# Kernel optimization log

Hardware: AMD Instinct MI355X
Metric: run time of the kernel (lower is better)

The kernel has to match this reference:

```python
import jax, jax.numpy as jnp
import numpy as np

D_MODEL = 1024
NUM_HEADS = 16
HEAD_DIM = D_MODEL // NUM_HEADS
BATCH = 2
SEQ = 2048


def setup_inputs() -> dict:
    key = jax.random.key(0)
    ks = jax.random.split(key, 9)
    s = 1.0 / np.sqrt(D_MODEL)
    X = jax.random.normal(ks[0], (BATCH, SEQ, D_MODEL), dtype=jnp.float32)
    # causal mask, broadcastable over batch and heads; masked_fill where mask == 0
    mask = jnp.tril(jnp.ones((SEQ, SEQ), dtype=jnp.int32))[None, None, :, :]
    Wq = jax.random.uniform(ks[1], (D_MODEL, D_MODEL), jnp.float32, -s, s)
    bq = jax.random.uniform(ks[2], (D_MODEL,), jnp.float32, -s, s)
    Wk = jax.random.uniform(ks[3], (D_MODEL, D_MODEL), jnp.float32, -s, s)
    bk = jax.random.uniform(ks[4], (D_MODEL,), jnp.float32, -s, s)
    Wv = jax.random.uniform(ks[5], (D_MODEL, D_MODEL), jnp.float32, -s, s)
    bv = jax.random.uniform(ks[6], (D_MODEL,), jnp.float32, -s, s)
    Wo = jax.random.uniform(ks[7], (D_MODEL, D_MODEL), jnp.float32, -s, s)
    bo = jax.random.uniform(ks[8], (D_MODEL,), jnp.float32, -s, s)
    return {"X": X, "mask": mask, "Wq": Wq, "bq": bq, "Wk": Wk, "bk": bk,
            "Wv": Wv, "bv": bv, "Wo": Wo, "bo": bo}


def reference(X, mask, Wq, bq, Wk, bk, Wv, bv, Wo, bo):
    B, S, _ = X.shape
    scale = 1.0 / np.sqrt(HEAD_DIM).astype(np.float32)

    def split_heads(t):  # [B,S,D] -> [B,H,S,Dh]
        return t.reshape(B, S, NUM_HEADS, HEAD_DIM).transpose(0, 2, 1, 3)

    q = split_heads(X @ Wq.T + bq)
    k = split_heads(X @ Wk.T + bk)
    v = split_heads(X @ Wv.T + bv)
    # [B,H,S,S] attention logits (explicitly materialized, as in the source)
    logits = jnp.einsum("bhqd,bhkd->bhqk", q, k) * scale
    logits = jnp.where(mask == 0, -jnp.inf, logits)
    attn = jax.nn.softmax(logits, axis=-1)  # dropout in eval mode: identity
    ctx = jnp.einsum("bhqk,bhkd->bhqd", attn, v)
    ctx = ctx.transpose(0, 2, 1, 3).reshape(B, S, D_MODEL)
    return ctx @ Wo.T + bo
```

## Files before the change

kernel.cpp:

```cpp
#include <hip/hip_runtime.h>


#define B_   2
#define S_   2048
#define H_   16
#define DH_  64
#define D_   1024
#define M_   (B_ * S_)

typedef __attribute__((ext_vector_type(8))) short short8;
typedef __attribute__((ext_vector_type(4))) short short4_t;
typedef float v4f __attribute__((ext_vector_type(4)));

__device__ __forceinline__ short f2bf(float f) {
    union { float f; unsigned u; } v; v.f = f;
    unsigned r = v.u + 0x7fffu + ((v.u >> 16) & 1u);
    return (short)(r >> 16);
}

#if __has_builtin(__builtin_amdgcn_exp2f)
#define EXP2(x) __builtin_amdgcn_exp2f(x)
#else
#define EXP2(x) exp2f(x)
#endif

__device__ __forceinline__ unsigned pack2(float a, float b) {
    return (__float_as_uint(a) >> 16) | (__float_as_uint(b) & 0xFFFF0000u);
}

__device__ __forceinline__ void gl2lds16(const short* g, short* l) {
    __builtin_amdgcn_global_load_lds(
        (const __attribute__((address_space(1))) unsigned int*)g,
        (__attribute__((address_space(3))) unsigned int*)l,
        16, 0, 0);
}

__global__ __launch_bounds__(256) void cast_kernel(
    const float* __restrict__ X,
    const float* __restrict__ Wq, const float* __restrict__ Wk,
    const float* __restrict__ Wv, const float* __restrict__ Wo,
    short* __restrict__ Xb, short* __restrict__ Wb)
{
    const int NX8 = (M_ * D_) / 8;
    const int NW8 = (D_ * D_) / 8;
    int idx = blockIdx.x * 256 + threadIdx.x;

    const float* src; short* dst; int off;
    if (idx < NX8) { src = X; dst = Xb; off = idx; }
    else {
        int r = idx - NX8;
        int sel = r >> 17;
        int o = r & (NW8 - 1);
        src = (sel == 0) ? Wq : (sel == 1) ? Wk : (sel == 2) ? Wv : Wo;
        dst = Wb + sel * (D_ * D_);
        off = o;
    }
    float4 f0 = ((const float4*)src)[off * 2];
    float4 f1 = ((const float4*)src)[off * 2 + 1];
    short8 s;
    s[0] = f2bf(f0.x); s[1] = f2bf(f0.y); s[2] = f2bf(f0.z); s[3] = f2bf(f0.w);
    s[4] = f2bf(f1.x); s[5] = f2bf(f1.y); s[6] = f2bf(f1.z); s[7] = f2bf(f1.w);
    *(short8*)(dst + (size_t)off * 8) = s;
}

template<int BN, int MODE>
__global__ __launch_bounds__(256) void gemm_kernel(
    const short* __restrict__ A, const short* __restrict__ W,
    const float* __restrict__ bq, const float* __restrict__ bk,
    const float* __restrict__ bv, void* __restrict__ out,
    int M, int N, int K)
{
    constexpr int SM = (MODE == 0) ? 18432 : (8192 + BN * 64);
    __shared__ __align__(16) short smem[SM];
    short* As = smem;
    short* Bs = smem + 8192;

    const int t    = threadIdx.x;
    const int lane = t & 63;
    const int wave = t >> 6;

    const int bid = blockIdx.x;
    const int by  = ((bid & 7) << 2) + ((bid >> 3) & 3);
    const int bx  = bid >> 5;
    const int m0 = by * 128;
    const int n0 = bx * BN;

    const int wm = (wave >> 1) * 64;
    const int wn = (wave & 1) * (BN / 2);
    constexpr int NJ  = BN / 32;
    constexpr int BIT = BN / 32;

    v4f acc[4][NJ] = {};

    const int rsub = lane >> 3;
    const int csw  = ((lane & 7) ^ rsub) * 8;
    const short* Ag = A + (size_t)(m0 + wave * 32 + rsub) * K + csw;
    const short* Wg = W + (size_t)(n0 + wave * (BN / 4) + rsub) * K + csw;
    short* Asw = As + (wave * 32) * 64;
    short* Bsw = Bs + (wave * (BN / 4)) * 64;

    const int lm = lane & 15;
    const int lg = lane >> 4;
    const int lm7 = lm & 7;

    for (int k0 = 0; k0 < K; k0 += 64) {
        #pragma unroll
        for (int i2 = 0; i2 < 4; ++i2)
            gl2lds16(Ag + (size_t)(i2 * 8) * K + k0, Asw + i2 * 512);
        #pragma unroll
        for (int i2 = 0; i2 < BIT; ++i2)
            gl2lds16(Wg + (size_t)(i2 * 8) * K + k0, Bsw + i2 * 512);
        __syncthreads();

        #pragma unroll
        for (int kk = 0; kk < 2; ++kk) {
            const int ch = (kk * 4 + lg) ^ lm7;
            short8 af[4], bf[NJ];
            #pragma unroll
            for (int i = 0; i < 4; ++i)
                af[i] = *(const short8*)((const char*)As + (wm + i * 16 + lm) * 128 + ch * 16);
            #pragma unroll
            for (int j = 0; j < NJ; ++j)
                bf[j] = *(const short8*)((const char*)Bs + (wn + j * 16 + lm) * 128 + ch * 16);
            #pragma unroll
            for (int i = 0; i < 4; ++i)
                #pragma unroll
                for (int j = 0; j < NJ; ++j)
                    acc[i][j] = __builtin_amdgcn_mfma_f32_16x16x32_bf16(af[i], bf[j], acc[i][j], 0, 0, 0);
        }
        __syncthreads();
    }

    const int sel = n0 >> 10;
    const float* bias = (MODE == 2) ? bq : (sel == 0) ? bq : (sel == 1) ? bk : bv;

    if constexpr (MODE == 2) {
        const int colb = n0 + wn + lm;
        const int rowb = m0 + wm + lg * 4;
        #pragma unroll
        for (int j = 0; j < NJ; ++j) {
            int col = colb + j * 16;
            float bv_ = bias[col];
            #pragma unroll
            for (int i = 0; i < 4; ++i)
                #pragma unroll
                for (int r = 0; r < 4; ++r)
                    ((float*)out)[(size_t)(rowb + i * 16 + r) * 1024 + col] = acc[i][j][r] + bv_;
        }
    } else {
        short* Es = smem + wave * (64 * 72);
        const int cb = (n0 + wn) & 1023;
        #pragma unroll
        for (int j = 0; j < 4; ++j) {
            float bv_ = bias[cb + j * 16 + lm];
            #pragma unroll
            for (int i = 0; i < 4; ++i)
                #pragma unroll
                for (int r = 0; r < 4; ++r) {
                    float vv = acc[i][j][r] + bv_;
                    if (sel == 0) vv *= 0.1803368867f;
                    if (sel < 2)
                        Es[(i * 16 + lg * 4 + r) * 72 + j * 16 + lm] = f2bf(vv);
                    else
                        Es[(j * 16 + lm) * 72 + i * 16 + lg * 4 + r] = f2bf(vv);
                }
        }
        __asm__ __volatile__("s_waitcnt lgkmcnt(0)" ::: "memory");
        short* outQKV = (short*)out;
        const int rl = lane >> 3;
        const int c8 = (lane & 7) * 8;
        const int h  = cb >> 6;
        const int b  = (m0 + wm) >> 11;
        const int bh = (b << 4) + h;
        if (sel < 2) {
            #pragma unroll
            for (int it = 0; it < 8; ++it) {
                int row_l = it * 8 + rl;
                short8 vrow = *(const short8*)&Es[row_l * 72 + c8];
                int s = (m0 + wm + row_l) & 2047;
                *(short8*)(outQKV + (size_t)sel * 4194304 +
                           ((size_t)bh * S_ + s) * DH_ + c8) = vrow;
            }
        } else {
            const int s0 = (m0 + wm) & 2047;
            #pragma unroll
            for (int it = 0; it < 8; ++it) {
                int d_l = it * 8 + rl;
                short8 vrow = *(const short8*)&Es[d_l * 72 + c8];
                *(short8*)(outQKV + (size_t)2 * 4194304 +
                           ((size_t)bh << 17) + ((size_t)d_l << 11) + s0 + c8) = vrow;
            }
        }
    }
}

__global__ __launch_bounds__(256, 2) void attn_kernel(
    const short* __restrict__ Q, const short* __restrict__ Kh,
    const short* __restrict__ Vt, short* __restrict__ ctx)
{
    __shared__ __align__(16) short sm[16384];
    short* Kt = sm;
    short* Vp = sm + 8192;

    const int t    = threadIdx.x;
    const int lane = t & 63;
    const int w    = t >> 6;
    const int bid  = blockIdx.x;

    const int lo  = bid & 255;
    const int xcd = lo & 7;
    const int idx = lo >> 3;
    const int bh  = (xcd << 2) + (idx & 3);
    const int jb  = idx >> 2;
    const int j   = (bid < 256) ? jb : (15 - jb);
    const int q0  = j * 128;
    const int npairs = j + 1;
    const int qr0 = q0 + w * 32;

    const int lm = lane & 15;
    const int lg = lane >> 4;

    const short* Qb = Q  + (size_t)bh * S_ * DH_;
    const short* Kb = Kh + (size_t)bh * S_ * DH_;
    const short* Vb = Vt + ((size_t)bh << 17);

    short8 qf[2][2];
    #pragma unroll
    for (int t2 = 0; t2 < 2; ++t2)
        #pragma unroll
        for (int kk = 0; kk < 2; ++kk)
            qf[t2][kk] = *(const short8*)(Qb + (size_t)(qr0 + t2 * 16 + lm) * DH_ + kk * 32 + lg * 8);

    float m_i[2] = {-1e30f, -1e30f}, l_i[2] = {0.f, 0.f};
    v4f o[2][4] = {};

    for (int it = 0; it < npairs; ++it) {
        const int kv0 = it * 128;
        const bool dpair = (it == npairs - 1);

        {
            const int rsub = lane >> 3;
            const int csw  = ((lane & 7) ^ rsub) * 8;
            #pragma unroll
            for (int i2 = 0; i2 < 4; ++i2) {
                const int rb = w * 32 + i2 * 8;
                gl2lds16(Kb + (size_t)(kv0 + rb + rsub) * 64 + csw, Kt + rb * 64);
            }
        }
        {
            const int d  = w * 16 + (lane >> 2);
            const int s3 = d & 7;
            short8 vld[4];
            #pragma unroll
            for (int m = 0; m < 4; ++m) {
                const int cm = (lane & 3) + 4 * m;
                vld[m] = *(const short8*)(Vb + (size_t)d * 2048 + kv0 + cm * 8);
            }
            char* vrow = (char*)Vp + d * 256;
            #pragma unroll
            for (int m = 0; m < 4; ++m) {
                const int cm = (lane & 3) + 4 * m;
                const int u  = cm >> 3, kk = (cm >> 2) & 1;
                const int q0off = ((cm & 1) << 4) + ((cm >> 1) & 1) * 4;
                const int bA = (u * 64 + kk * 32 + q0off) * 2;
                const int pA = ((((bA >> 4) ^ s3) << 4) | (bA & 15));
                const int bB = bA + 16;
                const int pB = ((((bB >> 4) ^ s3) << 4) | (bB & 15));
                *(short4_t*)(vrow + pA) = __builtin_shufflevector(vld[m], vld[m], 0, 1, 2, 3);
                *(short4_t*)(vrow + pB) = __builtin_shufflevector(vld[m], vld[m], 4, 5, 6, 7);
            }
        }
        __syncthreads();

        short8 vf[2][2][4];
        #pragma unroll
        for (int u = 0; u < 2; ++u)
            #pragma unroll
            for (int kk = 0; kk < 2; ++kk)
                #pragma unroll
                for (int i = 0; i < 4; ++i) {
                    const int d = i * 16 + lm;
                    const int ch = (u * 8 + kk * 4 + lg) ^ (lm & 7);
                    vf[u][kk][i] = *(const short8*)((const char*)Vp + d * 256 + ch * 16);
                }

        v4f sc[2][2][4] = {};
        #pragma unroll
        for (int u = 0; u < 2; ++u) {
            short8 kf[2][4];
            #pragma unroll
            for (int kk = 0; kk < 2; ++kk)
                #pragma unroll
                for (int jj = 0; jj < 4; ++jj) {
                    const int row = u * 64 + jj * 16 + lm;
                    const int ch  = (kk * 4 + lg) ^ (lm & 7);
                    kf[kk][jj] = *(const short8*)((const char*)Kt + row * 128 + ch * 16);
                }
            #pragma unroll
            for (int kk = 0; kk < 2; ++kk)
                #pragma unroll
                for (int t2 = 0; t2 < 2; ++t2)
                    #pragma unroll
                    for (int jj = 0; jj < 4; ++jj)
                        sc[t2][u][jj] = __builtin_amdgcn_mfma_f32_16x16x32_bf16(kf[kk][jj], qf[t2][kk], sc[t2][u][jj], 0, 0, 0);
        }

        float alpha[2];
        short8 pf[2][2][2];
        #pragma unroll
        for (int t2 = 0; t2 < 2; ++t2) {
            float x[2][4][4];
            const int q = qr0 + t2 * 16 + lm;
            #pragma unroll
            for (int u = 0; u < 2; ++u)
                #pragma unroll
                for (int jj = 0; jj < 4; ++jj)
                    #pragma unroll
                    for (int r = 0; r < 4; ++r) {
                        float v = sc[t2][u][jj][r];
                        if (dpair && (kv0 + u * 64 + jj * 16 + lg * 4 + r > q)) v = -1e30f;
                        x[u][jj][r] = v;
                    }
            float m8[8];
            #pragma unroll
            for (int z = 0; z < 8; ++z) {
                const float* xz = x[z >> 2][z & 3];
                m8[z] = fmaxf(fmaxf(xz[0], xz[1]), fmaxf(xz[2], xz[3]));
            }
            float rm = fmaxf(fmaxf(fmaxf(m8[0], m8[1]), fmaxf(m8[2], m8[3])),
                             fmaxf(fmaxf(m8[4], m8[5]), fmaxf(m8[6], m8[7])));
            rm = fmaxf(rm, __shfl_xor(rm, 16, 64));
            rm = fmaxf(rm, __shfl_xor(rm, 32, 64));

            const float mn = fmaxf(m_i[t2], rm);
            alpha[t2] = EXP2(m_i[t2] - mn);
            m_i[t2] = mn;

            float s8[8];
            #pragma unroll
            for (int z = 0; z < 8; ++z) {
                float* xz = x[z >> 2][z & 3];
                xz[0] = EXP2(xz[0] - mn); xz[1] = EXP2(xz[1] - mn);
                xz[2] = EXP2(xz[2] - mn); xz[3] = EXP2(xz[3] - mn);
                s8[z] = (xz[0] + xz[1]) + (xz[2] + xz[3]);
            }
            float rs = ((s8[0] + s8[1]) + (s8[2] + s8[3])) + ((s8[4] + s8[5]) + (s8[6] + s8[7]));
            rs += __shfl_xor(rs, 16, 64);
            rs += __shfl_xor(rs, 32, 64);
            l_i[t2] = l_i[t2] * alpha[t2] + rs;

            #pragma unroll
            for (int u = 0; u < 2; ++u)
                #pragma unroll
                for (int kk = 0; kk < 2; ++kk) {
                    union { short8 s; uint4 d; } pk;
                    pk.d.x = pack2(x[u][2 * kk][0],     x[u][2 * kk][1]);
                    pk.d.y = pack2(x[u][2 * kk][2],     x[u][2 * kk][3]);
                    pk.d.z = pack2(x[u][2 * kk + 1][0], x[u][2 * kk + 1][1]);
                    pk.d.w = pack2(x[u][2 * kk + 1][2], x[u][2 * kk + 1][3]);
                    pf[t2][u][kk] = pk.s;
                }
        }

        #pragma unroll
        for (int t2 = 0; t2 < 2; ++t2)
            #pragma unroll
            for (int i = 0; i < 4; ++i)
                o[t2][i] *= alpha[t2];

        #pragma unroll
        for (int u = 0; u < 2; ++u)
            #pragma unroll
            for (int kk = 0; kk < 2; ++kk)
                #pragma unroll
                for (int t2 = 0; t2 < 2; ++t2)
                    #pragma unroll
                    for (int i = 0; i < 4; ++i)
                        o[t2][i] = __builtin_amdgcn_mfma_f32_16x16x32_bf16(vf[u][kk][i], pf[t2][u][kk], o[t2][i], 0, 0, 0);

        __syncthreads();
    }

    const int b = bh >> 4, hd = bh & 15;
    #pragma unroll
    for (int t2 = 0; t2 < 2; ++t2) {
        const float inv = 1.f / l_i[t2];
        const size_t base = ((size_t)(b * S_ + qr0 + t2 * 16 + lm) << 10) + (hd << 6) + lg * 4;
        #pragma unroll
        for (int i = 0; i < 4; ++i) {
            short4_t s4;
            #pragma unroll
            for (int r = 0; r < 4; ++r) s4[r] = f2bf(o[t2][i][r] * inv);
            *(short4_t*)(ctx + base + i * 16) = s4;
        }
    }
}

extern "C" void kernel_launch(void* const* d_in, const int* in_sizes, int n_in,
                              void* d_out, int out_size, void* d_ws, size_t ws_size,
                              hipStream_t stream) {
    const float* X  = (const float*)d_in[0];
    const float* Wq = (const float*)d_in[2];
    const float* bq = (const float*)d_in[3];
    const float* Wk = (const float*)d_in[4];
    const float* bk = (const float*)d_in[5];
    const float* Wv = (const float*)d_in[6];
    const float* bv = (const float*)d_in[7];
    const float* Wo = (const float*)d_in[8];
    const float* bo = (const float*)d_in[9];
    float* out = (float*)d_out;

    short* ws  = (short*)d_ws;
    short* Xb  = ws;
    short* Wb  = Xb + 4194304;
    short* Qh  = Wb + 4194304;
    short* Kb  = Qh + 4194304;
    short* Vt  = Kb + 4194304;
    short* Ctx = Vt + 4194304;

    cast_kernel<<<4096, 256, 0, stream>>>(X, Wq, Wk, Wv, Wo, Xb, Wb);

    gemm_kernel<128, 0><<<768, 256, 0, stream>>>(
        Xb, Wb, bq, bk, bv, Qh, M_, 3 * D_, D_);

    attn_kernel<<<512, 256, 0, stream>>>(Qh, Kb, Vt, Ctx);

    gemm_kernel<64, 2><<<512, 256, 0, stream>>>(
        Ctx, Wb + 3145728, bo, bo, bo, out, M_, D_, D_);
}
```

Baseline: 195.8 us.

## Double-buffer K/V tiles in LDS to prefetch next block during compute

Doubles the attention kernel's shared memory to two K/V buffers and issues the next block's K async copy and V global loads before computing the current block. V is written into the alternate buffer after the MFMA work, so each iteration needs one barrier instead of two and load latency can overlap compute. The cost is 64KB of LDS per block, which may limit occupancy at 2 blocks per CU, plus extra registers held for the prefetched V.

```diff
diff --git a/kernel.cpp b/kernel.cpp
--- a/kernel.cpp
+++ b/kernel.cpp
@@ -198,9 +198,7 @@
     const short* __restrict__ Q, const short* __restrict__ Kh,
     const short* __restrict__ Vt, short* __restrict__ ctx)
 {
-    __shared__ __align__(16) short sm[16384];
-    short* Kt = sm;
-    short* Vp = sm + 8192;
+    __shared__ __align__(16) short sm[32768];
 
     const int t    = threadIdx.x;
     const int lane = t & 63;
@@ -224,6 +222,41 @@
     const short* Kb = Kh + (size_t)bh * S_ * DH_;
     const short* Vb = Vt + ((size_t)bh << 17);
 
+    const int rsubK = lane >> 3;
+    const int cswK  = ((lane & 7) ^ rsubK) * 8;
+    const int dV    = w * 16 + (lane >> 2);
+    const int s3V   = dV & 7;
+
+    auto stageK = [&](int kv0, short* Kt) {
+        #pragma unroll
+        for (int i2 = 0; i2 < 4; ++i2) {
+            const int rb = w * 32 + i2 * 8;
+            gl2lds16(Kb + (size_t)(kv0 + rb + rsubK) * 64 + cswK, Kt + rb * 64);
+        }
+    };
+    auto loadV = [&](int kv0, short8* vld) {
+        #pragma unroll
+        for (int m = 0; m < 4; ++m) {
+            const int cm = (lane & 3) + 4 * m;
+            vld[m] = *(const short8*)(Vb + (size_t)dV * 2048 + kv0 + cm * 8);
+        }
+    };
+    auto writeV = [&](const short8* vld, short* Vp) {
+        char* vrow = (char*)Vp + dV * 256;
+        #pragma unroll
+        for (int m = 0; m < 4; ++m) {
+            const int cm = (lane & 3) + 4 * m;
+            const int u  = cm >> 3, kk = (cm >> 2) & 1;
+            const int q0off = ((cm & 1) << 4) + ((cm >> 1) & 1) * 4;
+            const int bA = (u * 64 + kk * 32 + q0off) * 2;
+            const int pA = ((((bA >> 4) ^ s3V) << 4) | (bA & 15));
+            const int bB = bA + 16;
+            const int pB = ((((bB >> 4) ^ s3V) << 4) | (bB & 15));
+            *(short4_t*)(vrow + pA) = __builtin_shufflevector(vld[m], vld[m], 0, 1, 2, 3);
+            *(short4_t*)(vrow + pB) = __builtin_shufflevector(vld[m], vld[m], 4, 5, 6, 7);
+        }
+    };
+
     short8 qf[2][2];
     #pragma unroll
     for (int t2 = 0; t2 < 2; ++t2)
@@ -234,43 +267,26 @@
     float m_i[2] = {-1e30f, -1e30f}, l_i[2] = {0.f, 0.f};
     v4f o[2][4] = {};
 
+    short8 vpre[4];
+    stageK(0, sm);
+    loadV(0, vpre);
+    writeV(vpre, sm + 8192);
+    __syncthreads();
+
+    int cur = 0;
     for (int it = 0; it < npairs; ++it) {
         const int kv0 = it * 128;
         const bool dpair = (it == npairs - 1);
-
-        {
-            const int rsub = lane >> 3;
-            const int csw  = ((lane & 7) ^ rsub) * 8;
-            #pragma unroll
-            for (int i2 = 0; i2 < 4; ++i2) {
-                const int rb = w * 32 + i2 * 8;
-                gl2lds16(Kb + (size_t)(kv0 + rb + rsub) * 64 + csw, Kt + rb * 64);
-            }
-        }
-        {
-            const int d  = w * 16 + (lane >> 2);
-            const int s3 = d & 7;
-            short8 vld[4];
-            #pragma unroll
-            for (int m = 0; m < 4; ++m) {
-                const int cm = (lane & 3) + 4 * m;
-                vld[m] = *(const short8*)(Vb + (size_t)d * 2048 + kv0 + cm * 8);
-            }
-            char* vrow = (char*)Vp + d * 256;
-            #pragma unroll
-            for (int m = 0; m < 4; ++m) {
-                const int cm = (lane & 3) + 4 * m;
-                const int u  = cm >> 3, kk = (cm >> 2) & 1;
-                const int q0off = ((cm & 1) << 4) + ((cm >> 1) & 1) * 4;
-                const int bA = (u * 64 + kk * 32 + q0off) * 2;
-                const int pA = ((((bA >> 4) ^ s3) << 4) | (bA & 15));
-                const int bB = bA + 16;
-                const int pB = ((((bB >> 4) ^ s3) << 4) | (bB & 15));
-                *(short4_t*)(vrow + pA) = __builtin_shufflevector(vld[m], vld[m], 0, 1, 2, 3);
-                *(short4_t*)(vrow + pB) = __builtin_shufflevector(vld[m], vld[m], 4, 5, 6, 7);
-            }
-        }
-        __syncthreads();
+        const bool pre   = (it + 1 < npairs);
+        short* Kt  = sm + cur * 16384;
+        short* Vp  = Kt + 8192;
+        short* Ktn = sm + (cur ^ 1) * 16384;
+        short* Vpn = Ktn + 8192;
+
+        if (pre) {
+            stageK(kv0 + 128, Ktn);
+            loadV(kv0 + 128, vpre);
+        }
 
         short8 vf[2][2][4];
         #pragma unroll
@@ -378,7 +394,9 @@
                     for (int i = 0; i < 4; ++i)
                         o[t2][i] = __builtin_amdgcn_mfma_f32_16x16x32_bf16(vf[u][kk][i], pf[t2][u][kk], o[t2][i], 0, 0, 0);
 
+        if (pre) writeV(vpre, Vpn);
         __syncthreads();
+        cur ^= 1;
     }
 
     const int b = bh >> 4, hd = bh & 15;
```

Result: slower. 237.6 us (+21.4%).

## Split attention block across 8 waves with 16 query rows each

Applied to the files above, without the earlier changes.

The attention kernel now launches 512 threads (8 waves) per block instead of 256, and each wave handles 16 query rows instead of 32. The K and V tile loads into shared memory are redistributed across the 8 waves. This cuts per-thread registers and adds waves per CU to hide latency. In exchange, each wave re-reads the full K and V fragments from LDS for half as many queries, which doubles LDS read traffic per unit of work.

```diff
diff --git a/kernel.cpp b/kernel.cpp
--- a/kernel.cpp
+++ b/kernel.cpp
@@ -194,7 +194,7 @@
     }
 }
 
-__global__ __launch_bounds__(256, 2) void attn_kernel(
+__global__ __launch_bounds__(512, 2) void attn_kernel(
     const short* __restrict__ Q, const short* __restrict__ Kh,
     const short* __restrict__ Vt, short* __restrict__ ctx)
 {
@@ -215,7 +215,7 @@
     const int j   = (bid < 256) ? jb : (15 - jb);
     const int q0  = j * 128;
     const int npairs = j + 1;
-    const int qr0 = q0 + w * 32;
+    const int qr0 = q0 + w * 16;
 
     const int lm = lane & 15;
     const int lg = lane >> 4;
@@ -224,15 +224,13 @@
     const short* Kb = Kh + (size_t)bh * S_ * DH_;
     const short* Vb = Vt + ((size_t)bh << 17);
 
-    short8 qf[2][2];
+    short8 qf[2];
     #pragma unroll
-    for (int t2 = 0; t2 < 2; ++t2)
-        #pragma unroll
-        for (int kk = 0; kk < 2; ++kk)
-            qf[t2][kk] = *(const short8*)(Qb + (size_t)(qr0 + t2 * 16 + lm) * DH_ + kk * 32 + lg * 8);
-
-    float m_i[2] = {-1e30f, -1e30f}, l_i[2] = {0.f, 0.f};
-    v4f o[2][4] = {};
+    for (int kk = 0; kk < 2; ++kk)
+        qf[kk] = *(const short8*)(Qb + (size_t)(qr0 + lm) * DH_ + kk * 32 + lg * 8);
+
+    float m_i = -1e30f, l_i = 0.f;
+    v4f o[4] = {};
 
     for (int it = 0; it < npairs; ++it) {
         const int kv0 = it * 128;
@@ -242,24 +240,24 @@
             const int rsub = lane >> 3;
             const int csw  = ((lane & 7) ^ rsub) * 8;
             #pragma unroll
-            for (int i2 = 0; i2 < 4; ++i2) {
-                const int rb = w * 32 + i2 * 8;
+            for (int i2 = 0; i2 < 2; ++i2) {
+                const int rb = w * 16 + i2 * 8;
                 gl2lds16(Kb + (size_t)(kv0 + rb + rsub) * 64 + csw, Kt + rb * 64);
             }
         }
         {
-            const int d  = w * 16 + (lane >> 2);
+            const int d  = w * 8 + (lane >> 3);
             const int s3 = d & 7;
-            short8 vld[4];
-            #pragma unroll
-            for (int m = 0; m < 4; ++m) {
-                const int cm = (lane & 3) + 4 * m;
+            short8 vld[2];
+            #pragma unroll
+            for (int m = 0; m < 2; ++m) {
+                const int cm = (lane & 7) + 8 * m;
                 vld[m] = *(const short8*)(Vb + (size_t)d * 2048 + kv0 + cm * 8);
             }
             char* vrow = (char*)Vp + d * 256;
             #pragma unroll
-            for (int m = 0; m < 4; ++m) {
-                const int cm = (lane & 3) + 4 * m;
+            for (int m = 0; m < 2; ++m) {
+                const int cm = (lane & 7) + 8 * m;
                 const int u  = cm >> 3, kk = (cm >> 2) & 1;
                 const int q0off = ((cm & 1) << 4) + ((cm >> 1) & 1) * 4;
                 const int bA = (u * 64 + kk * 32 + q0off) * 2;
@@ -284,7 +282,7 @@
                     vf[u][kk][i] = *(const short8*)((const char*)Vp + d * 256 + ch * 16);
                 }
 
-        v4f sc[2][2][4] = {};
+        v4f sc[2][4] = {};
         #pragma unroll
         for (int u = 0; u < 2; ++u) {
             short8 kf[2][4];
@@ -299,25 +297,22 @@
             #pragma unroll
             for (int kk = 0; kk < 2; ++kk)
                 #pragma unroll
-                for (int t2 = 0; t2 < 2; ++t2)
-                    #pragma unroll
-                    for (int jj = 0; jj < 4; ++jj)
-                        sc[t2][u][jj] = __builtin_amdgcn_mfma_f32_16x16x32_bf16(kf[kk][jj], qf[t2][kk], sc[t2][u][jj], 0, 0, 0);
-        }
-
-        float alpha[2];
-        short8 pf[2][2][2];
-        #pragma unroll
-        for (int t2 = 0; t2 < 2; ++t2) {
+                for (int jj = 0; jj < 4; ++jj)
+                    sc[u][jj] = __builtin_amdgcn_mfma_f32_16x16x32_bf16(kf[kk][jj], qf[kk], sc[u][jj], 0, 0, 0);
+        }
+
+        float alpha;
+        short8 pf[2][2];
+        {
             float x[2][4][4];
-            const int q = qr0 + t2 * 16 + lm;
+            const int q = qr0 + lm;
             #pragma unroll
             for (int u = 0; u < 2; ++u)
                 #pragma unroll
                 for (int jj = 0; jj < 4; ++jj)
                     #pragma unroll
                     for (int r = 0; r < 4; ++r) {
-                        float v = sc[t2][u][jj][r];
+                        float v = sc[u][jj][r];
                         if (dpair && (kv0 + u * 64 + jj * 16 + lg * 4 + r > q)) v = -1e30f;
                         x[u][jj][r] = v;
                     }
@@ -332,9 +327,9 @@
             rm = fmaxf(rm, __shfl_xor(rm, 16, 64));
             rm = fmaxf(rm, __shfl_xor(rm, 32, 64));
 
-            const float mn = fmaxf(m_i[t2], rm);
-            alpha[t2] = EXP2(m_i[t2] - mn);
-            m_i[t2] = mn;
+            const float mn = fmaxf(m_i, rm);
+            alpha = EXP2(m_i - mn);
+            m_i = mn;
 
             float s8[8];
             #pragma unroll
@@ -347,7 +342,7 @@
             float rs = ((s8[0] + s8[1]) + (s8[2] + s8[3])) + ((s8[4] + s8[5]) + (s8[6] + s8[7]));
             rs += __shfl_xor(rs, 16, 64);
             rs += __shfl_xor(rs, 32, 64);
-            l_i[t2] = l_i[t2] * alpha[t2] + rs;
+            l_i = l_i * alpha + rs;
 
             #pragma unroll
             for (int u = 0; u < 2; ++u)
@@ -358,39 +353,34 @@
                     pk.d.y = pack2(x[u][2 * kk][2],     x[u][2 * kk][3]);
                     pk.d.z = pack2(x[u][2 * kk + 1][0], x[u][2 * kk + 1][1]);
                     pk.d.w = pack2(x[u][2 * kk + 1][2], x[u][2 * kk + 1][3]);
-                    pf[t2][u][kk] = pk.s;
+                    pf[u][kk] = pk.s;
                 }
         }
 
         #pragma unroll
-        for (int t2 = 0; t2 < 2; ++t2)
-            #pragma unroll
-            for (int i = 0; i < 4; ++i)
-                o[t2][i] *= alpha[t2];
+        for (int i = 0; i < 4; ++i)
+            o[i] *= alpha;
 
         #pragma unroll
         for (int u = 0; u < 2; ++u)
             #pragma unroll
             for (int kk = 0; kk < 2; ++kk)
                 #pragma unroll
-                for (int t2 = 0; t2 < 2; ++t2)
-                    #pragma unroll
-                    for (int i = 0; i < 4; ++i)
-                        o[t2][i] = __builtin_amdgcn_mfma_f32_16x16x32_bf16(vf[u][kk][i], pf[t2][u][kk], o[t2][i], 0, 0, 0);
+                for (int i = 0; i < 4; ++i)
+                    o[i] = __builtin_amdgcn_mfma_f32_16x16x32_bf16(vf[u][kk][i], pf[u][kk], o[i], 0, 0, 0);
 
         __syncthreads();
     }
 
     const int b = bh >> 4, hd = bh & 15;
-    #pragma unroll
-    for (int t2 = 0; t2 < 2; ++t2) {
-        const float inv = 1.f / l_i[t2];
-        const size_t base = ((size_t)(b * S_ + qr0 + t2 * 16 + lm) << 10) + (hd << 6) + lg * 4;
+    {
+        const float inv = 1.f / l_i;
+        const size_t base = ((size_t)(b * S_ + qr0 + lm) << 10) + (hd << 6) + lg * 4;
         #pragma unroll
         for (int i = 0; i < 4; ++i) {
             short4_t s4;
             #pragma unroll
-            for (int r = 0; r < 4; ++r) s4[r] = f2bf(o[t2][i][r] * inv);
+            for (int r = 0; r < 4; ++r) s4[r] = f2bf(o[i][r] * inv);
             *(short4_t*)(ctx + base + i * 16) = s4;
         }
     }
@@ -423,7 +413,7 @@
     gemm_kernel<128, 0><<<768, 256, 0, stream>>>(
         Xb, Wb, bq, bk, bv, Qh, M_, 3 * D_, D_);
 
-    attn_kernel<<<512, 256, 0, stream>>>(Qh, Kb, Vt, Ctx);
+    attn_kernel<<<512, 512, 0, stream>>>(Qh, Kb, Vt, Ctx);
 
     gemm_kernel<64, 2><<<512, 256, 0, stream>>>(
         Ctx, Wb + 3145728, bo, bo, bo, out, M_, D_, D_);
```

After: 191.1 us. 2.4% less time.

## Split attention KV range across two wave groups with in-block softmax merge

Applied to the files above, without the earlier changes.

The attention block grows from 256 to 512 threads. Two groups of four waves each process half of the causal KV tiles for the same 128 query rows, using separate shared-memory K/V buffers. At the end, group 1 writes its partial max, sum and output to LDS, and group 0 merges them with a log-sum-exp rescale before writing ctx. This doubles the waves working on each query tile to increase parallelism and latency hiding. In exchange it doubles LDS per block, may lower blocks per CU, and makes the inactive group idle at barriers when the tile count is odd.

```diff
diff --git a/kernel.cpp b/kernel.cpp
--- a/kernel.cpp
+++ b/kernel.cpp
@@ -194,17 +194,17 @@
     }
 }
 
-__global__ __launch_bounds__(256, 2) void attn_kernel(
+__global__ __launch_bounds__(512, 2) void attn_kernel(
     const short* __restrict__ Q, const short* __restrict__ Kh,
     const short* __restrict__ Vt, short* __restrict__ ctx)
 {
-    __shared__ __align__(16) short sm[16384];
-    short* Kt = sm;
-    short* Vp = sm + 8192;
+    __shared__ __align__(16) short sm[32768];
 
     const int t    = threadIdx.x;
     const int lane = t & 63;
     const int w    = t >> 6;
+    const int wg   = w & 3;
+    const int g    = w >> 2;
     const int bid  = blockIdx.x;
 
     const int lo  = bid & 255;
@@ -214,16 +214,28 @@
     const int jb  = idx >> 2;
     const int j   = (bid < 256) ? jb : (15 - jb);
     const int q0  = j * 128;
-    const int npairs = j + 1;
-    const int qr0 = q0 + w * 32;
+    const int nt  = j + 1;
+    const int ha  = nt >> 1;
+    const int mx  = nt - ha;
+    const int pb  = g ? ha : 0;
+    const int np  = g ? (nt - ha) : ha;
+    const int qr0 = q0 + wg * 32;
 
     const int lm = lane & 15;
     const int lg = lane >> 4;
+
+    short* Kt = sm + g * 16384;
+    short* Vp = Kt + 8192;
 
     const short* Qb = Q  + (size_t)bh * S_ * DH_;
     const short* Kb = Kh + (size_t)bh * S_ * DH_;
     const short* Vb = Vt + ((size_t)bh << 17);
 
+    const int rsubK = lane >> 3;
+    const int cswK  = ((lane & 7) ^ rsubK) * 8;
+    const int dV    = wg * 16 + (lane >> 2);
+    const int s3V   = dV & 7;
+
     short8 qf[2][2];
     #pragma unroll
     for (int t2 = 0; t2 < 2; ++t2)
@@ -234,164 +246,191 @@
     float m_i[2] = {-1e30f, -1e30f}, l_i[2] = {0.f, 0.f};
     v4f o[2][4] = {};
 
-    for (int it = 0; it < npairs; ++it) {
-        const int kv0 = it * 128;
-        const bool dpair = (it == npairs - 1);
-
-        {
-            const int rsub = lane >> 3;
-            const int csw  = ((lane & 7) ^ rsub) * 8;
+    for (int tI = 0; tI < mx; ++tI) {
+        const bool act   = tI < np;
+        const int  kv0   = (pb + tI) * 128;
+        const bool dpair = (g == 1) && (tI == mx - 1);
+
+        if (act) {
             #pragma unroll
             for (int i2 = 0; i2 < 4; ++i2) {
-                const int rb = w * 32 + i2 * 8;
-                gl2lds16(Kb + (size_t)(kv0 + rb + rsub) * 64 + csw, Kt + rb * 64);
-            }
-        }
-        {
-            const int d  = w * 16 + (lane >> 2);
-            const int s3 = d & 7;
+                const int rb = wg * 32 + i2 * 8;
+                gl2lds16(Kb + (size_t)(kv0 + rb + rsubK) * 64 + cswK, Kt + rb * 64);
+            }
             short8 vld[4];
             #pragma unroll
             for (int m = 0; m < 4; ++m) {
                 const int cm = (lane & 3) + 4 * m;
-                vld[m] = *(const short8*)(Vb + (size_t)d * 2048 + kv0 + cm * 8);
-            }
-            char* vrow = (char*)Vp + d * 256;
+                vld[m] = *(const short8*)(Vb + (size_t)dV * 2048 + kv0 + cm * 8);
+            }
+            char* vrow = (char*)Vp + dV * 256;
             #pragma unroll
             for (int m = 0; m < 4; ++m) {
                 const int cm = (lane & 3) + 4 * m;
                 const int u  = cm >> 3, kk = (cm >> 2) & 1;
                 const int q0off = ((cm & 1) << 4) + ((cm >> 1) & 1) * 4;
                 const int bA = (u * 64 + kk * 32 + q0off) * 2;
-                const int pA = ((((bA >> 4) ^ s3) << 4) | (bA & 15));
+                const int pA = ((((bA >> 4) ^ s3V) << 4) | (bA & 15));
                 const int bB = bA + 16;
-                const int pB = ((((bB >> 4) ^ s3) << 4) | (bB & 15));
+                const int pB = ((((bB >> 4) ^ s3V) << 4) | (bB & 15));
                 *(short4_t*)(vrow + pA) = __builtin_shufflevector(vld[m], vld[m], 0, 1, 2, 3);
                 *(short4_t*)(vrow + pB) = __builtin_shufflevector(vld[m], vld[m], 4, 5, 6, 7);
             }
         }
         __syncthreads();
 
-        short8 vf[2][2][4];
-        #pragma unroll
-        for (int u = 0; u < 2; ++u)
-            #pragma unroll
-            for (int kk = 0; kk < 2; ++kk)
-                #pragma unroll
-                for (int i = 0; i < 4; ++i) {
-                    const int d = i * 16 + lm;
-                    const int ch = (u * 8 + kk * 4 + lg) ^ (lm & 7);
-                    vf[u][kk][i] = *(const short8*)((const char*)Vp + d * 256 + ch * 16);
+        if (act) {
+            short8 vf[2][2][4];
+            #pragma unroll
+            for (int u = 0; u < 2; ++u)
+                #pragma unroll
+                for (int kk = 0; kk < 2; ++kk)
+                    #pragma unroll
+                    for (int i = 0; i < 4; ++i) {
+                        const int d = i * 16 + lm;
+                        const int ch = (u * 8 + kk * 4 + lg) ^ (lm & 7);
+                        vf[u][kk][i] = *(const short8*)((const char*)Vp + d * 256 + ch * 16);
+                    }
+
+            v4f sc[2][2][4] = {};
+            #pragma unroll
+            for (int u = 0; u < 2; ++u) {
+                short8 kf[2][4];
+                #pragma unroll
+                for (int kk = 0; kk < 2; ++kk)
+                    #pragma unroll
+                    for (int jj = 0; jj < 4; ++jj) {
+                        const int row = u * 64 + jj * 16 + lm;
+                        const int ch  = (kk * 4 + lg) ^ (lm & 7);
+                        kf[kk][jj] = *(const short8*)((const char*)Kt + row * 128 + ch * 16);
+                    }
+                #pragma unroll
+                for (int kk = 0; kk < 2; ++kk)
+                    #pragma unroll
+                    for (int t2 = 0; t2 < 2; ++t2)
+                        #pragma unroll
+                        for (int jj = 0; jj < 4; ++jj)
+                            sc[t2][u][jj] = __builtin_amdgcn_mfma_f32_16x16x32_bf16(kf[kk][jj], qf[t2][kk], sc[t2][u][jj], 0, 0, 0);
+            }
+
+            float alpha[2];
+            short8 pf[2][2][2];
+            #pragma unroll
+            for (int t2 = 0; t2 < 2; ++t2) {
+                float x[2][4][4];
+                const int q = qr0 + t2 * 16 + lm;
+                #pragma unroll
+                for (int u = 0; u < 2; ++u)
+                    #pragma unroll
+                    for (int jj = 0; jj < 4; ++jj)
+                        #pragma unroll
+                        for (int r = 0; r < 4; ++r) {
+                            float v = sc[t2][u][jj][r];
+                            if (dpair && (kv0 + u * 64 + jj * 16 + lg * 4 + r > q)) v = -1e30f;
+                            x[u][jj][r] = v;
+                        }
+                float m8[8];
+                #pragma unroll
+                for (int z = 0; z < 8; ++z) {
+                    const float* xz = x[z >> 2][z & 3];
+                    m8[z] = fmaxf(fmaxf(xz[0], xz[1]), fmaxf(xz[2], xz[3]));
                 }
-
-        v4f sc[2][2][4] = {};
-        #pragma unroll
-        for (int u = 0; u < 2; ++u) {
-            short8 kf[2][4];
-            #pragma unroll
-            for (int kk = 0; kk < 2; ++kk)
-                #pragma unroll
-                for (int jj = 0; jj < 4; ++jj) {
-                    const int row = u * 64 + jj * 16 + lm;
-                    const int ch  = (kk * 4 + lg) ^ (lm & 7);
-                    kf[kk][jj] = *(const short8*)((const char*)Kt + row * 128 + ch * 16);
+                float rm = fmaxf(fmaxf(fmaxf(m8[0], m8[1]), fmaxf(m8[2], m8[3])),
+                                 fmaxf(fmaxf(m8[4], m8[5]), fmaxf(m8[6], m8[7])));
+                rm = fmaxf(rm, __shfl_xor(rm, 16, 64));
+                rm = fmaxf(rm, __shfl_xor(rm, 32, 64));
+
+                const float mn = fmaxf(m_i[t2], rm);
+                alpha[t2] = EXP2(m_i[t2] - mn);
+                m_i[t2] = mn;
+
+                float s8[8];
+                #pragma unroll
+                for (int z = 0; z < 8; ++z) {
+                    float* xz = x[z >> 2][z & 3];
+                    xz[0] = EXP2(xz[0] - mn); xz[1] = EXP2(xz[1] - mn);
+                    xz[2] = EXP2(xz[2] - mn); xz[3] = EXP2(xz[3] - mn);
+                    s8[z] = (xz[0] + xz[1]) + (xz[2] + xz[3]);
                 }
-            #pragma unroll
-            for (int kk = 0; kk < 2; ++kk)
-                #pragma unroll
-                for (int t2 = 0; t2 < 2; ++t2)
-                    #pragma unroll
-                    for (int jj = 0; jj < 4; ++jj)
-                        sc[t2][u][jj] = __builtin_amdgcn_mfma_f32_16x16x32_bf16(kf[kk][jj], qf[t2][kk], sc[t2][u][jj], 0, 0, 0);
-        }
-
-        float alpha[2];
-        short8 pf[2][2][2];
+                float rs = ((s8[0] + s8[1]) + (s8[2] + s8[3])) + ((s8[4] + s8[5]) + (s8[6] + s8[7]));
+                rs += __shfl_xor(rs, 16, 64);
+                rs += __shfl_xor(rs, 32, 64);
+                l_i[t2] = l_i[t2] * alpha[t2] + rs;
+
+                #pragma unroll
+                for (int u = 0; u < 2; ++u)
+                    #pragma unroll
+                    for (int kk = 0; kk < 2; ++kk) {
+                        union { short8 s; uint4 d; } pk;
+                        pk.d.x = pack2(x[u][2 * kk][0],     x[u][2 * kk][1]);
+                        pk.d.y = pack2(x[u][2 * kk][2],     x[u][2 * kk][3]);
+                        pk.d.z = pack2(x[u][2 * kk + 1][0], x[u][2 * kk + 1][1]);
+                        pk.d.w = pack2(x[u][2 * kk + 1][2], x[u][2 * kk + 1][3]);
+                        pf[t2][u][kk] = pk.s;
+                    }
+            }
+
+            #pragma unroll
+            for (int t2 = 0; t2 < 2; ++t2)
+                #pragma unroll
+                for (int i = 0; i < 4; ++i)
+                    o[t2][i] *= alpha[t2];
+
+            #pragma unroll
+            for (int u = 0; u < 2; ++u)
+                #pragma unroll
+                for (int kk = 0; kk < 2; ++kk)
+                    #pragma unroll
+                    for (int t2 = 0; t2 < 2; ++t2)
+                        #pragma unroll
+                        for (int i = 0; i < 4; ++i)
+                            o[t2][i] = __builtin_amdgcn_mfma_f32_16x16x32_bf16(vf[u][kk][i], pf[t2][u][kk], o[t2][i], 0, 0, 0);
+        }
+        __syncthreads();
+    }
+
+    float* fb = (float*)sm;
+    if (g == 1) {
+        float* mp = &fb[(wg * 64 + lane) * 36];
+        mp[0] = m_i[0]; mp[1] = l_i[0]; mp[2] = m_i[1]; mp[3] = l_i[1];
+        #pragma unroll
+        for (int t2 = 0; t2 < 2; ++t2)
+            #pragma unroll
+            for (int i = 0; i < 4; ++i)
+                #pragma unroll
+                for (int r = 0; r < 4; ++r)
+                    mp[4 + t2 * 16 + i * 4 + r] = o[t2][i][r];
+    }
+    __syncthreads();
+    if (g == 0) {
+        const float* mp = &fb[(wg * 64 + lane) * 36];
         #pragma unroll
         for (int t2 = 0; t2 < 2; ++t2) {
-            float x[2][4][4];
-            const int q = qr0 + t2 * 16 + lm;
-            #pragma unroll
-            for (int u = 0; u < 2; ++u)
-                #pragma unroll
-                for (int jj = 0; jj < 4; ++jj)
-                    #pragma unroll
-                    for (int r = 0; r < 4; ++r) {
-                        float v = sc[t2][u][jj][r];
-                        if (dpair && (kv0 + u * 64 + jj * 16 + lg * 4 + r > q)) v = -1e30f;
-                        x[u][jj][r] = v;
-                    }
-            float m8[8];
-            #pragma unroll
-            for (int z = 0; z < 8; ++z) {
-                const float* xz = x[z >> 2][z & 3];
-                m8[z] = fmaxf(fmaxf(xz[0], xz[1]), fmaxf(xz[2], xz[3]));
-            }
-            float rm = fmaxf(fmaxf(fmaxf(m8[0], m8[1]), fmaxf(m8[2], m8[3])),
-                             fmaxf(fmaxf(m8[4], m8[5]), fmaxf(m8[6], m8[7])));
-            rm = fmaxf(rm, __shfl_xor(rm, 16, 64));
-            rm = fmaxf(rm, __shfl_xor(rm, 32, 64));
-
-            const float mn = fmaxf(m_i[t2], rm);
-            alpha[t2] = EXP2(m_i[t2] - mn);
-            m_i[t2] = mn;
-
-            float s8[8];
-            #pragma unroll
-            for (int z = 0; z < 8; ++z) {
-                float* xz = x[z >> 2][z & 3];
-                xz[0] = EXP2(xz[0] - mn); xz[1] = EXP2(xz[1] - mn);
-                xz[2] = EXP2(xz[2] - mn); xz[3] = EXP2(xz[3] - mn);
-                s8[z] = (xz[0] + xz[1]) + (xz[2] + xz[3]);
-            }
-            float rs = ((s8[0] + s8[1]) + (s8[2] + s8[3])) + ((s8[4] + s8[5]) + (s8[6] + s8[7]));
-            rs += __shfl_xor(rs, 16, 64);
-            rs += __shfl_xor(rs, 32, 64);
-            l_i[t2] = l_i[t2] * alpha[t2] + rs;
-
-            #pragma unroll
-            for (int u = 0; u < 2; ++u)
-                #pragma unroll
-                for (int kk = 0; kk < 2; ++kk) {
-                    union { short8 s; uint4 d; } pk;
-                    pk.d.x = pack2(x[u][2 * kk][0],     x[u][2 * kk][1]);
-                    pk.d.y = pack2(x[u][2 * kk][2],     x[u][2 * kk][3]);
-                    pk.d.z = pack2(x[u][2 * kk + 1][0], x[u][2 * kk + 1][1]);
-                    pk.d.w = pack2(x[u][2 * kk + 1][2], x[u][2 * kk + 1][3]);
-                    pf[t2][u][kk] = pk.s;
-                }
-        }
-
-        #pragma unroll
-        for (int t2 = 0; t2 < 2; ++t2)
-            #pragma unroll
-            for (int i = 0; i < 4; ++i)
-                o[t2][i] *= alpha[t2];
-
-        #pragma unroll
-        for (int u = 0; u < 2; ++u)
-            #pragma unroll
-            for (int kk = 0; kk < 2; ++kk)
-                #pragma unroll
-                for (int t2 = 0; t2 < 2; ++t2)
-                    #pragma unroll
-                    for (int i = 0; i < 4; ++i)
-                        o[t2][i] = __builtin_amdgcn_mfma_f32_16x16x32_bf16(vf[u][kk][i], pf[t2][u][kk], o[t2][i], 0, 0, 0);
-
-        __syncthreads();
-    }
-
-    const int b = bh >> 4, hd = bh & 15;
-    #pragma unroll
-    for (int t2 = 0; t2 < 2; ++t2) {
-        const float inv = 1.f / l_i[t2];
-        const size_t base = ((size_t)(b * S_ + qr0 + t2 * 16 + lm) << 10) + (hd << 6) + lg * 4;
-        #pragma unroll
-        for (int i = 0; i < 4; ++i) {
-            short4_t s4;
-            #pragma unroll
-            for (int r = 0; r < 4; ++r) s4[r] = f2bf(o[t2][i][r] * inv);
-            *(short4_t*)(ctx + base + i * 16) = s4;
+            const float mo = mp[t2 * 2];
+            const float lo = mp[t2 * 2 + 1];
+            const float mn = fmaxf(m_i[t2], mo);
+            const float sa = EXP2(m_i[t2] - mn);
+            const float sb = EXP2(mo - mn);
+            l_i[t2] = l_i[t2] * sa + lo * sb;
+            #pragma unroll
+            for (int i = 0; i < 4; ++i)
+                #pragma unroll
+                for (int r = 0; r < 4; ++r)
+                    o[t2][i][r] = o[t2][i][r] * sa + mp[4 + t2 * 16 + i * 4 + r] * sb;
+        }
+
+        const int b = bh >> 4, hd = bh & 15;
+        #pragma unroll
+        for (int t2 = 0; t2 < 2; ++t2) {
+            const float inv = 1.f / l_i[t2];
+            const size_t base = ((size_t)(b * S_ + qr0 + t2 * 16 + lm) << 10) + (hd << 6) + lg * 4;
+            #pragma unroll
+            for (int i = 0; i < 4; ++i) {
+                short4_t s4;
+                #pragma unroll
+                for (int r = 0; r < 4; ++r) s4[r] = f2bf(o[t2][i][r] * inv);
+                *(short4_t*)(ctx + base + i * 16) = s4;
+            }
         }
     }
 }
@@ -423,7 +462,7 @@
     gemm_kernel<128, 0><<<768, 256, 0, stream>>>(
         Xb, Wb, bq, bk, bv, Qh, M_, 3 * D_, D_);
 
-    attn_kernel<<<512, 256, 0, stream>>>(Qh, Kb, Vt, Ctx);
+    attn_kernel<<<512, 512, 0, stream>>>(Qh, Kb, Vt, Ctx);
 
     gemm_kernel<64, 2><<<512, 256, 0, stream>>>(
         Ctx, Wb + 3145728, bo, bo, bo, out, M_, D_, D_);
```

Result: no change. 193.1 us (-1.3%).
